# Kernel optimization log

Hardware: AMD Instinct MI355X
Metric: run time of the kernel (lower is better)

## Reference

```python
import jax, jax.numpy as jnp
import numpy as np

N_NODES = 50000
N_HYPEREDGES = 50000
E = 320000
D = 256


def _prelu(x, a):
    return jnp.where(x >= 0, x, a * x)


def _hypergraph_conv(x, hei, W, b, num_nodes, num_edges):
    # PyG HypergraphConv, use_attention=False, heads=1:
    # out = D^{-1} H B^{-1} H^T (X W^T) + b
    src = hei[0]  # node indices, [E]
    he = hei[1]   # hyperedge indices, [E]
    xw = x @ W.T  # [N, D] node transform (lin has no bias)
    ones = jnp.ones((hei.shape[1],), x.dtype)
    deg_n = jax.ops.segment_sum(ones, src, num_segments=num_nodes)   # node degree D
    deg_e = jax.ops.segment_sum(ones, he, num_segments=num_edges)    # hyperedge size B
    d_inv = jnp.where(deg_n > 0, 1.0 / deg_n, 0.0)
    b_inv = jnp.where(deg_e > 0, 1.0 / deg_e, 0.0)
    # node -> hyperedge aggregation, scaled by B^{-1}
    edge_feat = b_inv[:, None] * jax.ops.segment_sum(xw[src], he, num_segments=num_edges)  # [n_he, D]
    # hyperedge -> node aggregation, scaled by D^{-1}
    out = d_inv[:, None] * jax.ops.segment_sum(edge_feat[he], src, num_segments=num_nodes)  # [N, D]
    return out + b


def setup_inputs() -> dict:
    key = jax.random.key(0)
    ks = jax.random.split(key, 6)
    std = np.sqrt(2.0 / D)  # kaiming_normal
    x = jax.random.normal(ks[0], (N_NODES, D), dtype=jnp.float32)
    hyper_edge_index = jax.random.randint(ks[1], (2, E), 0, N_HYPEREDGES, dtype=jnp.int64)
    W1 = jax.random.normal(ks[2], (D, D), dtype=jnp.float32) * std
    b1 = jnp.zeros((D,), jnp.float32)
    W2 = jax.random.normal(ks[3], (D, D), dtype=jnp.float32) * std
    b2 = jnp.zeros((D,), jnp.float32)
    prelu_a = jnp.asarray(0.25, jnp.float32)
    return {"x": x, "W1": W1, "b1": b1, "W2": W2, "b2": b2,
            "prelu_a": prelu_a, "hyper_edge_index": hyper_edge_index}


def reference(x, W1, b1, W2, b2, prelu_a, hyper_edge_index):
    out = _hypergraph_conv(x, hyper_edge_index, W1, b1, N_NODES, N_HYPEREDGES)
    out = _prelu(out, prelu_a)
    out = _hypergraph_conv(out, hyper_edge_index, W2, b2, N_NODES, N_HYPEREDGES)
    out = out + x  # residual
    out = _prelu(out, prelu_a)
    return out
```

## Files before the change

kernel.cpp:

```cpp
#include <hip/hip_runtime.h>

#define NN    50000
#define NHE   50000
#define NEDGE 320000
#define DD    256

#define SB    1024
#define NBLK  ((NN + SB - 1) / SB)

typedef float f32x4 __attribute__((ext_vector_type(4)));
typedef short short8 __attribute__((ext_vector_type(8)));

static __device__ __forceinline__ unsigned short f2b(float f) {
    union { float f; unsigned u; } c; c.f = f;
    unsigned u = c.u;
    u += 0x7fffu + ((u >> 16) & 1u);
    return (unsigned short)(u >> 16);
}
static __device__ __forceinline__ float b2f_lo(unsigned v) {
    union { unsigned u; float f; } c; c.u = v << 16; return c.f;
}
static __device__ __forceinline__ float b2f_hi(unsigned v) {
    union { unsigned u; float f; } c; c.u = v & 0xffff0000u; return c.f;
}
static __device__ __forceinline__ unsigned pack2(float a, float b) {
    return (unsigned)f2b(a) | ((unsigned)f2b(b) << 16);
}

static __device__ __forceinline__ void glds16(const unsigned short* g, unsigned short* l) {
    __builtin_amdgcn_global_load_lds((const __attribute__((address_space(1))) unsigned int*)g,
                                     (__attribute__((address_space(3))) unsigned int*)l,
                                     16, 0, 0);
}

__global__ __launch_bounds__(256) void k_count(const int* __restrict__ src,
                                               const int* __restrict__ he,
                                               int* __restrict__ cnt_n,
                                               int* __restrict__ cnt_e) {
    int e = blockIdx.x * 256 + threadIdx.x;
    if (e >= NEDGE) return;
    atomicAdd(&cnt_n[src[e]], 1);
    atomicAdd(&cnt_e[he[e]], 1);
}

__global__ __launch_bounds__(256) void k_scan_a(const int* __restrict__ cnt_n,
                                                const int* __restrict__ cnt_e,
                                                int* __restrict__ bsum) {
    int b   = blockIdx.x;
    int seg = b / NBLK, lb = b % NBLK;
    const int* cnt = seg ? cnt_e : cnt_n;
    int t = threadIdx.x;
    int idx = lb * SB + t * 4;
    int s = 0;
#pragma unroll
    for (int j = 0; j < 4; ++j)
        if (idx + j < NN) s += cnt[idx + j];
    __shared__ int red[256];
    red[t] = s;
    __syncthreads();
    for (int o = 128; o > 0; o >>= 1) {
        if (t < o) red[t] += red[t + o];
        __syncthreads();
    }
    if (t == 0) bsum[b] = red[0];
}

__global__ __launch_bounds__(64) void k_scan_b(const int* __restrict__ bsum,
                                               int* __restrict__ bbase) {
    if (threadIdx.x == 0) {
        int r = 0;
        for (int i = 0; i < NBLK; ++i) { bbase[i] = r; r += bsum[i]; }
        bbase[2 * NBLK] = r;
        r = 0;
        for (int i = NBLK; i < 2 * NBLK; ++i) { bbase[i] = r; r += bsum[i]; }
        bbase[2 * NBLK + 1] = r;
    }
}

__global__ __launch_bounds__(256) void k_scan_c(const int* __restrict__ cnt_n,
                                                const int* __restrict__ cnt_e,
                                                const int* __restrict__ bbase,
                                                int* __restrict__ off_n,
                                                int* __restrict__ off_e,
                                                int* __restrict__ cur_n,
                                                int* __restrict__ cur_e) {
    int b   = blockIdx.x;
    int seg = b / NBLK, lb = b % NBLK;
    const int* cnt = seg ? cnt_e : cnt_n;
    int* off = seg ? off_e : off_n;
    int* cur = seg ? cur_e : cur_n;
    int t = threadIdx.x;
    int idx = lb * SB + t * 4;
    int v[4];
    int tsum = 0;
#pragma unroll
    for (int j = 0; j < 4; ++j) {
        v[j] = (idx + j < NN) ? cnt[idx + j] : 0;
        tsum += v[j];
    }
    __shared__ int sc[256];
    sc[t] = tsum;
    __syncthreads();
    for (int o = 1; o < 256; o <<= 1) {
        int val = (t >= o) ? sc[t - o] : 0;
        __syncthreads();
        sc[t] += val;
        __syncthreads();
    }
    int p = bbase[b] + sc[t] - tsum;
#pragma unroll
    for (int j = 0; j < 4; ++j) {
        if (idx + j < NN) { off[idx + j] = p; cur[idx + j] = 0; }
        p += v[j];
    }
    if (b == 0 && t == 0) off_n[NN] = bbase[2 * NBLK];
    if (b == NBLK && t == 0) off_e[NHE] = bbase[2 * NBLK + 1];
}

__global__ __launch_bounds__(256) void k_fill(const int* __restrict__ src,
                                              const int* __restrict__ he,
                                              const int* __restrict__ off_n,
                                              const int* __restrict__ off_e,
                                              int* __restrict__ cur_n,
                                              int* __restrict__ cur_e,
                                              int* __restrict__ adj_n,
                                              int* __restrict__ adj_e) {
    int e = blockIdx.x * 256 + threadIdx.x;
    if (e >= NEDGE) return;
    int s = src[e], h = he[e];
    int pn = off_n[s] + atomicAdd(&cur_n[s], 1);
    adj_n[pn] = h;
    int pe = off_e[h] + atomicAdd(&cur_e[h], 1);
    adj_e[pe] = s;
}

__global__ __launch_bounds__(256) void k_cvt_w(const float* __restrict__ w1,
                                               const float* __restrict__ w2,
                                               unsigned short* __restrict__ o1,
                                               unsigned short* __restrict__ o2) {
    int t = blockIdx.x * 256 + threadIdx.x;
    const int n4 = DD * DD / 4;
    const float* s = (t < n4) ? w1 : w2;
    unsigned short* d = (t < n4) ? o1 : o2;
    int i = (t < n4) ? t : t - n4;
    float4 v = ((const float4*)s)[i];
    uint2 o;
    o.x = pack2(v.x, v.y);
    o.y = pack2(v.z, v.w);
    ((uint2*)d)[i] = o;
}

template <bool A32>
__global__ __launch_bounds__(256) void k_gemm128(const void* __restrict__ Av,
                                                 const unsigned short* __restrict__ Wb,
                                                 unsigned short* __restrict__ Cb, int M) {
    __shared__ __align__(16) unsigned short As[128 * 32];
    __shared__ __align__(16) unsigned short Bs[128 * 32];
    const int t    = threadIdx.x;
    const int m0   = blockIdx.x * 128;
    const int n0   = blockIdx.y * 128;
    const int lane = t & 63;
    const int wave = t >> 6;
    const int wm   = (wave >> 1) * 64;
    const int wn   = (wave & 1) * 64;
    const int fr   = lane & 15;
    const int fq   = lane >> 4;

    f32x4 acc[4][4] = {};

    const int rl0 = wave * 32 + (lane >> 2);
    const int ar = t >> 1;
    const int ah = t & 1;

    for (int k0 = 0; k0 < DD; k0 += 32) {
        __syncthreads();
#pragma unroll
        for (int q = 0; q < 2; ++q) {
            int rl = rl0 + q * 16;
            int c  = (lane & 3) ^ (rl & 3);
            glds16(Wb + (size_t)(n0 + rl) * DD + k0 + c * 8,
                   Bs + (size_t)(wave * 32 + q * 16) * 32);
        }
        if (A32) {
            int gr = m0 + ar; if (gr >= M) gr = M - 1;
            const float* p = (const float*)Av + (size_t)gr * DD + k0 + ah * 16;
            float4 f0 = ((const float4*)p)[0];
            float4 f1 = ((const float4*)p)[1];
            float4 f2 = ((const float4*)p)[2];
            float4 f3 = ((const float4*)p)[3];
            uint4 u0, u1;
            u0.x = pack2(f0.x, f0.y); u0.y = pack2(f0.z, f0.w);
            u0.z = pack2(f1.x, f1.y); u0.w = pack2(f1.z, f1.w);
            u1.x = pack2(f2.x, f2.y); u1.y = pack2(f2.z, f2.w);
            u1.z = pack2(f3.x, f3.y); u1.w = pack2(f3.z, f3.w);
            int p0 = (2 * ah) ^ (ar & 3);
            int p1 = (2 * ah + 1) ^ (ar & 3);
            *(uint4*)(As + ar * 32 + p0 * 8) = u0;
            *(uint4*)(As + ar * 32 + p1 * 8) = u1;
        } else {
#pragma unroll
            for (int q = 0; q < 2; ++q) {
                int rl = rl0 + q * 16;
                int gr = m0 + rl; if (gr >= M) gr = M - 1;
                int c  = (lane & 3) ^ (rl & 3);
                glds16((const unsigned short*)Av + (size_t)gr * DD + k0 + c * 8,
                       As + (size_t)(wave * 32 + q * 16) * 32);
            }
        }
        __syncthreads();

        short8 af[4], bf[4];
#pragma unroll
        for (int mt = 0; mt < 4; ++mt) {
            int r = wm + mt * 16 + fr;
            af[mt] = *(const short8*)(As + r * 32 + ((fq ^ (r & 3)) * 8));
        }
#pragma unroll
        for (int nt = 0; nt < 4; ++nt) {
            int r = wn + nt * 16 + fr;
            bf[nt] = *(const short8*)(Bs + r * 32 + ((fq ^ (r & 3)) * 8));
        }
#pragma unroll
        for (int mt = 0; mt < 4; ++mt)
#pragma unroll
            for (int nt = 0; nt < 4; ++nt)
                acc[mt][nt] = __builtin_amdgcn_mfma_f32_16x16x32_bf16(af[mt], bf[nt],
                                                                      acc[mt][nt], 0, 0, 0);
    }

#pragma unroll
    for (int mt = 0; mt < 4; ++mt) {
#pragma unroll
        for (int i = 0; i < 4; ++i) {
            int gm = m0 + wm + mt * 16 + fq * 4 + i;
            if (gm >= M) continue;
#pragma unroll
            for (int nt = 0; nt < 4; ++nt) {
                int gn = n0 + wn + nt * 16 + fr;
                Cb[(size_t)gm * DD + gn] = f2b(acc[mt][nt][i]);
            }
        }
    }
}

static __device__ __forceinline__ void acc8(float* a, uint4 v) {
    a[0] += b2f_lo(v.x); a[1] += b2f_hi(v.x);
    a[2] += b2f_lo(v.y); a[3] += b2f_hi(v.y);
    a[4] += b2f_lo(v.z); a[5] += b2f_hi(v.z);
    a[6] += b2f_lo(v.w); a[7] += b2f_hi(v.w);
}
static __device__ __forceinline__ void gather8(const unsigned short* __restrict__ srcb,
                                               const int* __restrict__ adj,
                                               int b, int e, int sl, float* a) {
#pragma unroll
    for (int i = 0; i < 8; ++i) a[i] = 0.f;
    for (int i = b; i < e; i += 8) {
        int g0 = adj[i];
        int g[8];
        g[0] = g0;
#pragma unroll
        for (int j = 1; j < 8; ++j) g[j] = (i + j < e) ? adj[i + j] : g0;
        uint4 v[8];
#pragma unroll
        for (int j = 0; j < 8; ++j)
            v[j] = *(const uint4*)(srcb + (size_t)g[j] * DD + sl * 8);
        acc8(a, v[0]);
#pragma unroll
        for (int j = 1; j < 8; ++j)
            if (i + j < e) acc8(a, v[j]);
    }
}

__global__ __launch_bounds__(256) void k_gather_edge_b(const unsigned short* __restrict__ xw,
                                                       unsigned short* __restrict__ ef,
                                                       const int* __restrict__ off,
                                                       const int* __restrict__ adj) {
    int tid = blockIdx.x * 256 + threadIdx.x;
    int w = tid >> 5;
    int sl = tid & 31;
    if (w >= NHE) return;
    int b = off[w], e = off[w + 1];
    float a[8];
    gather8(xw, adj, b, e, sl, a);
    float sc = (e > b) ? 1.f / (float)(e - b) : 0.f;
    uint4 o;
    o.x = pack2(a[0] * sc, a[1] * sc);
    o.y = pack2(a[2] * sc, a[3] * sc);
    o.z = pack2(a[4] * sc, a[5] * sc);
    o.w = pack2(a[6] * sc, a[7] * sc);
    *(uint4*)(ef + (size_t)w * DD + sl * 8) = o;
}

__global__ __launch_bounds__(256) void k_gather_node_mid_b(const unsigned short* __restrict__ ef,
                                                           unsigned short* __restrict__ h,
                                                           const int* __restrict__ off,
                                                           const int* __restrict__ adj,
                                                           const float* __restrict__ bias,
                                                           const float* __restrict__ aP) {
    int tid = blockIdx.x * 256 + threadIdx.x;
    int w = tid >> 5;
    int sl = tid & 31;
    if (w >= NN) return;
    int b = off[w], e = off[w + 1];
    float a[8];
    gather8(ef, adj, b, e, sl, a);
    float sc = (e > b) ? 1.f / (float)(e - b) : 0.f;
    float al = *aP;
    float4 bb0 = ((const float4*)bias)[sl * 2];
    float4 bb1 = ((const float4*)bias)[sl * 2 + 1];
    float r[8];
    r[0] = a[0] * sc + bb0.x; r[1] = a[1] * sc + bb0.y;
    r[2] = a[2] * sc + bb0.z; r[3] = a[3] * sc + bb0.w;
    r[4] = a[4] * sc + bb1.x; r[5] = a[5] * sc + bb1.y;
    r[6] = a[6] * sc + bb1.z; r[7] = a[7] * sc + bb1.w;
#pragma unroll
    for (int i = 0; i < 8; ++i) r[i] = (r[i] >= 0.f) ? r[i] : al * r[i];
    uint4 o;
    o.x = pack2(r[0], r[1]);
    o.y = pack2(r[2], r[3]);
    o.z = pack2(r[4], r[5]);
    o.w = pack2(r[6], r[7]);
    *(uint4*)(h + (size_t)w * DD + sl * 8) = o;
}

__global__ __launch_bounds__(256) void k_gather_node_final_b(const unsigned short* __restrict__ ef,
                                                             const float* __restrict__ x,
                                                             float* __restrict__ out,
                                                             const int* __restrict__ off,
                                                             const int* __restrict__ adj,
                                                             const float* __restrict__ bias,
                                                             const float* __restrict__ aP) {
    int tid = blockIdx.x * 256 + threadIdx.x;
    int w = tid >> 5;
    int sl = tid & 31;
    if (w >= NN) return;
    int b = off[w], e = off[w + 1];
    float a[8];
    gather8(ef, adj, b, e, sl, a);
    float sc = (e > b) ? 1.f / (float)(e - b) : 0.f;
    float al = *aP;
    float4 bb0 = ((const float4*)bias)[sl * 2];
    float4 bb1 = ((const float4*)bias)[sl * 2 + 1];
    const float* xp = x + (size_t)w * DD + sl * 8;
    float4 xv0 = *(const float4*)xp;
    float4 xv1 = *(const float4*)(xp + 4);
    float r[8];
    r[0] = a[0] * sc + bb0.x + xv0.x; r[1] = a[1] * sc + bb0.y + xv0.y;
    r[2] = a[2] * sc + bb0.z + xv0.z; r[3] = a[3] * sc + bb0.w + xv0.w;
    r[4] = a[4] * sc + bb1.x + xv1.x; r[5] = a[5] * sc + bb1.y + xv1.y;
    r[6] = a[6] * sc + bb1.z + xv1.z; r[7] = a[7] * sc + bb1.w + xv1.w;
#pragma unroll
    for (int i = 0; i < 8; ++i) r[i] = (r[i] >= 0.f) ? r[i] : al * r[i];
    float* op = out + (size_t)w * DD + sl * 8;
    *(float4*)op = make_float4(r[0], r[1], r[2], r[3]);
    *(float4*)(op + 4) = make_float4(r[4], r[5], r[6], r[7]);
}

extern "C" void kernel_launch(void* const* d_in, const int* in_sizes, int n_in,
                              void* d_out, int out_size, void* d_ws, size_t ws_size,
                              hipStream_t stream) {
    const float* x       = (const float*)d_in[0];
    const float* W1      = (const float*)d_in[1];
    const float* b1      = (const float*)d_in[2];
    const float* W2      = (const float*)d_in[3];
    const float* b2      = (const float*)d_in[4];
    const float* prelu_a = (const float*)d_in[5];
    const int*   hei     = (const int*)d_in[6];
    const int* idx_src = hei;
    const int* idx_he  = hei + NEDGE;

    float* out = (float*)d_out;
    unsigned short* B1 = (unsigned short*)d_ws;
    unsigned short* B2 = B1 + (size_t)NN * DD;
    int* off_n = (int*)(B2 + (size_t)NN * DD);
    int* off_e = off_n + NN + 1;
    int* cur_n = off_e + NHE + 1;
    int* cur_e = cur_n + NN;
    int* adj_n = cur_e + NHE;
    int* adj_e = adj_n + NEDGE;
    int* bsum  = adj_e + NEDGE;
    int* bbase = bsum + 2 * NBLK;
    unsigned short* w1b = (unsigned short*)d_out;
    unsigned short* w2b = w1b + DD * DD;

    const int eblocks = (NEDGE + 255) / 256;
    const int gblocks = (NN * 32 + 255) / 256;
    dim3 ggrid((NN + 127) / 128, DD / 128);

    hipMemsetAsync(cur_n, 0, sizeof(int) * (NN + NHE), stream);
    k_count<<<eblocks, 256, 0, stream>>>(idx_src, idx_he, cur_n, cur_e);
    k_scan_a<<<2 * NBLK, 256, 0, stream>>>(cur_n, cur_e, bsum);
    k_scan_b<<<1, 64, 0, stream>>>(bsum, bbase);
    k_scan_c<<<2 * NBLK, 256, 0, stream>>>(cur_n, cur_e, bbase, off_n, off_e,
                                           cur_n, cur_e);
    k_fill<<<eblocks, 256, 0, stream>>>(idx_src, idx_he, off_n, off_e,
                                        cur_n, cur_e, adj_n, adj_e);

    k_cvt_w<<<(2 * DD * DD / 4 + 255) / 256, 256, 0, stream>>>(W1, W2, w1b, w2b);

    k_gemm128<true><<<ggrid, 256, 0, stream>>>((const void*)x, w1b, B1, NN);
    k_gather_edge_b<<<gblocks, 256, 0, stream>>>(B1, B2, off_e, adj_e);
    k_gather_node_mid_b<<<gblocks, 256, 0, stream>>>(B2, B1, off_n, adj_n, b1, prelu_a);

    k_gemm128<false><<<ggrid, 256, 0, stream>>>((const void*)B1, w2b, B2, NN);
    k_gather_edge_b<<<gblocks, 256, 0, stream>>>(B2, B1, off_e, adj_e);
    k_gather_node_final_b<<<gblocks, 256, 0, stream>>>(B1, x, out, off_n, adj_n, b2, prelu_a);
}
```

Baseline: 335.6 us.

## Record atomic ranks in count pass, drop fill atomics, fuse weight conversion

The count kernel now keeps the return value of each atomicAdd as a per-edge rank, so the fill kernel writes adjacency entries at offset plus rank without a second round of atomics. The cursor reset is removed, and count and fill each handle four edges per thread using int4 loads. The bf16 weight conversion is folded into extra blocks of the scan_a kernel, which removes one launch. The cost is two extra rank arrays of size E in workspace and the extra memory traffic to write and read them.

```diff
diff --git a/kernel.cpp b/kernel.cpp
--- a/kernel.cpp
+++ b/kernel.cpp
@@ -36,17 +36,48 @@
 __global__ __launch_bounds__(256) void k_count(const int* __restrict__ src,
                                                const int* __restrict__ he,
                                                int* __restrict__ cnt_n,
-                                               int* __restrict__ cnt_e) {
-    int e = blockIdx.x * 256 + threadIdx.x;
-    if (e >= NEDGE) return;
-    atomicAdd(&cnt_n[src[e]], 1);
-    atomicAdd(&cnt_e[he[e]], 1);
+                                               int* __restrict__ cnt_e,
+                                               int* __restrict__ rank_n,
+                                               int* __restrict__ rank_e) {
+    int t  = blockIdx.x * 256 + threadIdx.x;
+    int e0 = t * 4;
+    if (e0 >= NEDGE) return;
+    int4 s = *(const int4*)(src + e0);
+    int4 h = *(const int4*)(he + e0);
+    int4 rn, re;
+    rn.x = atomicAdd(&cnt_n[s.x], 1);
+    rn.y = atomicAdd(&cnt_n[s.y], 1);
+    rn.z = atomicAdd(&cnt_n[s.z], 1);
+    rn.w = atomicAdd(&cnt_n[s.w], 1);
+    re.x = atomicAdd(&cnt_e[h.x], 1);
+    re.y = atomicAdd(&cnt_e[h.y], 1);
+    re.z = atomicAdd(&cnt_e[h.z], 1);
+    re.w = atomicAdd(&cnt_e[h.w], 1);
+    *(int4*)(rank_n + e0) = rn;
+    *(int4*)(rank_e + e0) = re;
 }
 
 __global__ __launch_bounds__(256) void k_scan_a(const int* __restrict__ cnt_n,
                                                 const int* __restrict__ cnt_e,
-                                                int* __restrict__ bsum) {
-    int b   = blockIdx.x;
+                                                int* __restrict__ bsum,
+                                                const float* __restrict__ w1,
+                                                const float* __restrict__ w2,
+                                                unsigned short* __restrict__ o1,
+                                                unsigned short* __restrict__ o2) {
+    int b = blockIdx.x;
+    if (b >= 2 * NBLK) {
+        int t = (b - 2 * NBLK) * 256 + threadIdx.x;
+        const int n4 = DD * DD / 4;
+        const float* s = (t < n4) ? w1 : w2;
+        unsigned short* d = (t < n4) ? o1 : o2;
+        int i = (t < n4) ? t : t - n4;
+        float4 v = ((const float4*)s)[i];
+        uint2 o;
+        o.x = pack2(v.x, v.y);
+        o.y = pack2(v.z, v.w);
+        ((uint2*)d)[i] = o;
+        return;
+    }
     int seg = b / NBLK, lb = b % NBLK;
     const int* cnt = seg ? cnt_e : cnt_n;
     int t = threadIdx.x;
@@ -81,14 +112,11 @@
                                                 const int* __restrict__ cnt_e,
                                                 const int* __restrict__ bbase,
                                                 int* __restrict__ off_n,
-                                                int* __restrict__ off_e,
-                                                int* __restrict__ cur_n,
-                                                int* __restrict__ cur_e) {
+                                                int* __restrict__ off_e) {
     int b   = blockIdx.x;
     int seg = b / NBLK, lb = b % NBLK;
     const int* cnt = seg ? cnt_e : cnt_n;
     int* off = seg ? off_e : off_n;
-    int* cur = seg ? cur_e : cur_n;
     int t = threadIdx.x;
     int idx = lb * SB + t * 4;
     int v[4];
@@ -110,7 +138,7 @@
     int p = bbase[b] + sc[t] - tsum;
 #pragma unroll
     for (int j = 0; j < 4; ++j) {
-        if (idx + j < NN) { off[idx + j] = p; cur[idx + j] = 0; }
+        if (idx + j < NN) off[idx + j] = p;
         p += v[j];
     }
     if (b == 0 && t == 0) off_n[NN] = bbase[2 * NBLK];
@@ -121,33 +149,27 @@
                                               const int* __restrict__ he,
                                               const int* __restrict__ off_n,
                                               const int* __restrict__ off_e,
-                                              int* __restrict__ cur_n,
-                                              int* __restrict__ cur_e,
+                                              const int* __restrict__ rank_n,
+                                              const int* __restrict__ rank_e,
                                               int* __restrict__ adj_n,
                                               int* __restrict__ adj_e) {
-    int e = blockIdx.x * 256 + threadIdx.x;
-    if (e >= NEDGE) return;
-    int s = src[e], h = he[e];
-    int pn = off_n[s] + atomicAdd(&cur_n[s], 1);
-    adj_n[pn] = h;
-    int pe = off_e[h] + atomicAdd(&cur_e[h], 1);
-    adj_e[pe] = s;
-}
-
-__global__ __launch_bounds__(256) void k_cvt_w(const float* __restrict__ w1,
-                                               const float* __restrict__ w2,
-                                               unsigned short* __restrict__ o1,
-                                               unsigned short* __restrict__ o2) {
-    int t = blockIdx.x * 256 + threadIdx.x;
-    const int n4 = DD * DD / 4;
-    const float* s = (t < n4) ? w1 : w2;
-    unsigned short* d = (t < n4) ? o1 : o2;
-    int i = (t < n4) ? t : t - n4;
-    float4 v = ((const float4*)s)[i];
-    uint2 o;
-    o.x = pack2(v.x, v.y);
-    o.y = pack2(v.z, v.w);
-    ((uint2*)d)[i] = o;
+    int t  = blockIdx.x * 256 + threadIdx.x;
+    int e0 = t * 4;
+    if (e0 >= NEDGE) return;
+    int4 s  = *(const int4*)(src + e0);
+    int4 h  = *(const int4*)(he + e0);
+    int4 rn = *(const int4*)(rank_n + e0);
+    int4 re = *(const int4*)(rank_e + e0);
+    int on0 = off_n[s.x], on1 = off_n[s.y], on2 = off_n[s.z], on3 = off_n[s.w];
+    int oe0 = off_e[h.x], oe1 = off_e[h.y], oe2 = off_e[h.z], oe3 = off_e[h.w];
+    adj_n[on0 + rn.x] = h.x;
+    adj_n[on1 + rn.y] = h.y;
+    adj_n[on2 + rn.z] = h.z;
+    adj_n[on3 + rn.w] = h.w;
+    adj_e[oe0 + re.x] = s.x;
+    adj_e[oe1 + re.y] = s.y;
+    adj_e[oe2 + re.z] = s.z;
+    adj_e[oe3 + re.w] = s.w;
 }
 
 template <bool A32>
@@ -372,31 +394,32 @@
     float* out = (float*)d_out;
     unsigned short* B1 = (unsigned short*)d_ws;
     unsigned short* B2 = B1 + (size_t)NN * DD;
-    int* off_n = (int*)(B2 + (size_t)NN * DD);
-    int* off_e = off_n + NN + 1;
-    int* cur_n = off_e + NHE + 1;
-    int* cur_e = cur_n + NN;
-    int* adj_n = cur_e + NHE;
-    int* adj_e = adj_n + NEDGE;
-    int* bsum  = adj_e + NEDGE;
-    int* bbase = bsum + 2 * NBLK;
+    int* off_n  = (int*)(B2 + (size_t)NN * DD);
+    int* off_e  = off_n + NN + 1;
+    int* cnt_n  = off_e + NHE + 1;
+    int* cnt_e  = cnt_n + NN;
+    int* adj_n  = cnt_e + NHE;
+    int* adj_e  = adj_n + NEDGE;
+    int* rank_n = adj_e + NEDGE;
+    int* rank_e = rank_n + NEDGE;
+    int* bsum   = rank_e + NEDGE;
+    int* bbase  = bsum + 2 * NBLK;
     unsigned short* w1b = (unsigned short*)d_out;
     unsigned short* w2b = w1b + DD * DD;
 
-    const int eblocks = (NEDGE + 255) / 256;
+    const int e4blocks = (NEDGE / 4 + 255) / 256;
     const int gblocks = (NN * 32 + 255) / 256;
     dim3 ggrid((NN + 127) / 128, DD / 128);
 
-    hipMemsetAsync(cur_n, 0, sizeof(int) * (NN + NHE), stream);
-    k_count<<<eblocks, 256, 0, stream>>>(idx_src, idx_he, cur_n, cur_e);
-    k_scan_a<<<2 * NBLK, 256, 0, stream>>>(cur_n, cur_e, bsum);
+    hipMemsetAsync(cnt_n, 0, sizeof(int) * (NN + NHE), stream);
+    k_count<<<e4blocks, 256, 0, stream>>>(idx_src, idx_he, cnt_n, cnt_e,
+                                          rank_n, rank_e);
+    k_scan_a<<<2 * NBLK + 128, 256, 0, stream>>>(cnt_n, cnt_e, bsum,
+                                                 W1, W2, w1b, w2b);
     k_scan_b<<<1, 64, 0, stream>>>(bsum, bbase);
-    k_scan_c<<<2 * NBLK, 256, 0, stream>>>(cur_n, cur_e, bbase, off_n, off_e,
-                                           cur_n, cur_e);
-    k_fill<<<eblocks, 256, 0, stream>>>(idx_src, idx_he, off_n, off_e,
-                                        cur_n, cur_e, adj_n, adj_e);
-
-    k_cvt_w<<<(2 * DD * DD / 4 + 255) / 256, 256, 0, stream>>>(W1, W2, w1b, w2b);
+    k_scan_c<<<2 * NBLK, 256, 0, stream>>>(cnt_n, cnt_e, bbase, off_n, off_e);
+    k_fill<<<e4blocks, 256, 0, stream>>>(idx_src, idx_he, off_n, off_e,
+                                         rank_n, rank_e, adj_n, adj_e);
 
     k_gemm128<true><<<ggrid, 256, 0, stream>>>((const void*)x, w1b, B1, NN);
     k_gather_edge_b<<<gblocks, 256, 0, stream>>>(B1, B2, off_e, adj_e);
```

Result: faster. 308.9 us (-8.0%).
